# Optimization experiments

Measured on AMD Instinct MI355X. Metric: run time of the kernel, lower is better.

## Reference

```python
import jax, jax.numpy as jnp
import numpy as np

N = 131072      # points (rays x samples chunk)
E = 8           # spatial sub-networks (centroids)
DIN = 90        # encoded pos+dir features fed to sub-NeRFs (xyz_real=True -> x[:, 3:])
H = 256         # sub-NeRF hidden width
DOUT = 4        # rgb + sigma
MARGIN = 2.0    # boundary_margin
EPS = 1e-8


def setup_inputs() -> dict:
    key = jax.random.key(0)
    k = jax.random.split(key, 5)
    x_xyz = jax.random.uniform(k[0], (N, 3), dtype=jnp.float32)          # routing coords in [0,1)^3
    x_feat = jax.random.normal(k[1], (N, DIN), dtype=jnp.float32)        # encoded features
    x = jnp.concatenate([x_xyz, x_feat], axis=1)                         # [N, 3+DIN]
    centroids = jax.random.uniform(k[2], (E, 3), dtype=jnp.float32)
    W1 = jax.random.normal(k[3], (E, DIN, H), dtype=jnp.float32) * 0.05
    b1 = jnp.zeros((E, H), dtype=jnp.float32)
    W2 = jax.random.normal(k[4], (E, H, DOUT), dtype=jnp.float32) * 0.05
    b2 = jnp.zeros((E, DOUT), dtype=jnp.float32)
    return {"x": x, "centroids": centroids, "W1": W1, "b1": b1, "W2": W2, "b2": b2}


def reference(x, centroids, W1, b1, W2, b2):
    # --- centroid routing (torch.cdist equivalent) ---
    xyz = x[:, :3]                                                       # [N,3]
    d2 = jnp.sum((xyz[:, None, :] - centroids[None, :, :]) ** 2, axis=-1)
    dist = jnp.sqrt(jnp.maximum(d2, 0.0))                                # [N,E]
    inv = 1.0 / (dist + EPS)
    min_d = jnp.min(dist, axis=1, keepdims=True)                         # [N,1]
    inv = jnp.where(dist > MARGIN * min_d, 0.0, inv)                     # zero far experts
    weights = inv / jnp.sum(inv, axis=-1, keepdims=True)                 # [N,E], rows sum to 1

    # --- per-expert sub-NeRF MLP, weighted combine ---
    # Dense-equivalent of masked gather + weighted scatter-add: experts whose
    # weight is exactly 0 contribute nothing, matching the torch masked path.
    feat = x[:, 3:]                                                      # xyz_real=True -> drop xyz
    h = jax.nn.relu(jnp.einsum('nd,edh->enh', feat, W1) + b1[:, None, :])  # [E,N,H]
    out_e = jnp.einsum('enh,eho->eno', h, W2) + b2[:, None, :]             # [E,N,DOUT]
    return jnp.einsum('eno,ne->no', out_e, weights)                        # [N,DOUT]
```

## Files before the change

kernel.cpp:

```cpp
#include <hip/hip_runtime.h>

#define NPTS 131072
#define NE 8
#define DIN 90
#define NH 256

typedef __attribute__((ext_vector_type(8))) short bf16x8;
typedef __attribute__((ext_vector_type(4))) float f32x4;
typedef __attribute__((ext_vector_type(2))) float f32x2;
typedef __attribute__((ext_vector_type(4))) unsigned int u32x4;
typedef __attribute__((ext_vector_type(2))) unsigned int u32x2;
typedef __attribute__((ext_vector_type(4), aligned(4))) float f32x4a;
typedef __attribute__((ext_vector_type(2), aligned(4))) float f32x2a;

__device__ __forceinline__ unsigned short f2bf(float f) {
  unsigned int u = __float_as_uint(f);
  u += 0x7fffu + ((u >> 16) & 1u);
  return (unsigned short)(u >> 16);
}

#if defined(__has_builtin) && __has_builtin(__builtin_amdgcn_cvt_pk_bf16_f32)
typedef __attribute__((ext_vector_type(2))) __bf16 bf16x2;
__device__ __forceinline__ unsigned int pkbf(float f0, float f1) {
  bf16x2 r = __builtin_amdgcn_cvt_pk_bf16_f32(f0, f1);
  return __builtin_bit_cast(unsigned int, r);
}
#else
__device__ __forceinline__ unsigned int pkbf(float f0, float f1) {
  unsigned int u0 = __float_as_uint(f0) + 0x7fffu;
  unsigned int u1 = __float_as_uint(f1) + 0x7fffu;
  return __builtin_amdgcn_perm(u1, u0, 0x07060302u);
}
#endif

__device__ __forceinline__ bf16x8 cvt8(f32x4 a, f32x4 b) {
  u32x4 r;
  r[0] = pkbf(a[0], a[1]);
  r[1] = pkbf(a[2], a[3]);
  r[2] = pkbf(b[0], b[1]);
  r[3] = pkbf(b[2], b[3]);
  return __builtin_bit_cast(bf16x8, r);
}

#define PREP_T (184320 + 12288 + 8192 + 24576)
__global__ __launch_bounds__(256) void prep(const float* __restrict__ W1,
                                            const float* __restrict__ W2,
                                            unsigned short* __restrict__ W1T,
                                            unsigned short* __restrict__ W2T) {
  int tid = blockIdx.x * 256 + threadIdx.x;
  if (tid < 184320) {
    float v = W1[tid];
    int n = tid & 255, r = tid >> 8;
    int kp = r % 90, e = r / 90;
    W1T[(size_t)(e * NH + n) * 96 + kp] = f2bf(v);
    return;
  }
  tid -= 184320;
  if (tid < 12288) {
    int kp = 90 + tid % 6, q = tid / 6;
    int n = q & 255, e = q >> 8;
    W1T[(size_t)(e * NH + n) * 96 + kp] = 0;
    return;
  }
  tid -= 12288;
  if (tid < 8192) {
    float v = W2[tid];
    int o = tid & 3, k = (tid >> 2) & 255, e = tid >> 10;
    W2T[(size_t)(e * 16 + o) * NH + k] = f2bf(v);
    return;
  }
  tid -= 8192;
  if (tid < 24576) {
    int k = tid & 255, q = tid >> 8;
    int o = 4 + q % 12, e = q / 12;
    W2T[(size_t)(e * 16 + o) * NH + k] = 0;
  }
}

__global__ __launch_bounds__(256, 3) void meganerf_main(
    const float* __restrict__ x, const float* __restrict__ cent,
    const float* __restrict__ b1, const float* __restrict__ b2,
    const unsigned short* __restrict__ W1T, const unsigned short* __restrict__ W2T,
    float* __restrict__ out) {
  __shared__ unsigned short sH[4 * 2048];
  __shared__ float sW[NE][64];
  __shared__ float sB2[64][4];
  __shared__ float sB1[NE * NH];

  const int t    = threadIdx.x;
  const int lane = t & 63;
  const int wid  = t >> 6;
  const int l15  = lane & 15;
  const int l4   = lane >> 4;
  const int row0 = blockIdx.x * 64;
  const int gbase = wid * 2048;

#pragma unroll
  for (int j = 0; j < 2; ++j)
    *(f32x4*)&sB1[t * 4 + j * 1024] = *(const f32x4a*)&b1[t * 4 + j * 1024];

  bf16x8 bfr[4][3];
#pragma unroll
  for (int nf = 0; nf < 4; ++nf) {
    const float* gr = x + (size_t)(row0 + 16 * nf + l15) * 93 + 3;
    f32x4 v0, v1;
    v0 = *(const f32x4a*)(gr + 8 * l4);
    v1 = *(const f32x4a*)(gr + 8 * l4 + 4);
    bfr[nf][0] = cvt8(v0, v1);
    v0 = *(const f32x4a*)(gr + 32 + 8 * l4);
    v1 = *(const f32x4a*)(gr + 36 + 8 * l4);
    bfr[nf][1] = cvt8(v0, v1);
    if (l4 < 3) {
      v0 = *(const f32x4a*)(gr + 64 + 8 * l4);
      v1 = *(const f32x4a*)(gr + 68 + 8 * l4);
    } else {
      f32x2 tl = *(const f32x2a*)(gr + 88);
      v0[0] = tl[0]; v0[1] = tl[1]; v0[2] = 0.f; v0[3] = 0.f;
      v1[0] = 0.f; v1[1] = 0.f; v1[2] = 0.f; v1[3] = 0.f;
    }
    bfr[nf][2] = cvt8(v0, v1);
  }

  if (t < 64) {
    const float* gx = x + (size_t)(row0 + t) * 93;
    float px = gx[0], py = gx[1], pz = gx[2];
    float dist[NE], inv[NE];
    float mind = 3.4e38f;
#pragma unroll
    for (int e = 0; e < NE; ++e) {
      float dx = px - cent[e * 3 + 0];
      float dy = py - cent[e * 3 + 1];
      float dz = pz - cent[e * 3 + 2];
      float d2 = dx * dx + dy * dy + dz * dz;
      float d = sqrtf(fmaxf(d2, 0.f));
      dist[e] = d;
      inv[e] = 1.f / (d + 1e-8f);
      mind = fminf(mind, d);
    }
    float s = 0.f;
#pragma unroll
    for (int e = 0; e < NE; ++e) {
      if (dist[e] > 2.0f * mind) inv[e] = 0.f;
      s += inv[e];
    }
    float rs = 1.f / s;
    float bb[4] = {0.f, 0.f, 0.f, 0.f};
#pragma unroll
    for (int e = 0; e < NE; ++e) {
      float w = inv[e] * rs;
      sW[e][t] = w;
#pragma unroll
      for (int o = 0; o < 4; ++o) bb[o] += w * b2[e * 4 + o];
    }
#pragma unroll
    for (int o = 0; o < 4; ++o) sB2[t][o] = bb[o];
  }
  __syncthreads();

  bf16x8 w1buf[2][6];
  bf16x8 bwbuf[2];
  float wv[4];

  auto loadW1 = [&](int idx, int buf) {
    const int e = idx >> 1, c = idx & 1;
    const unsigned short* p =
        W1T + (size_t)(e * NH + 128 * c + 32 * wid + l15) * 96 + 8 * l4;
#pragma unroll
    for (int mf = 0; mf < 2; ++mf)
#pragma unroll
      for (int ks = 0; ks < 3; ++ks)
        w1buf[buf][mf * 3 + ks] = *(const bf16x8*)(p + mf * (16 * 96) + 32 * ks);
  };
  auto loadBW = [&](int idx, int buf) {
    const int e = idx >> 1, c = idx & 1;
    bwbuf[buf] = *(const bf16x8*)(W2T + (size_t)(e * 16 + l15) * NH +
                                  128 * c + 32 * wid + 8 * l4);
  };

  loadBW(0, 0);
  loadW1(0, 0);

  f32x4 facc[4] = {{0.f, 0.f, 0.f, 0.f}, {0.f, 0.f, 0.f, 0.f},
                   {0.f, 0.f, 0.f, 0.f}, {0.f, 0.f, 0.f, 0.f}};

#pragma unroll 2
  for (int i = 0; i < 16; ++i) {
    const int e = i >> 1, c = i & 1, cur = i & 1, nxt = cur ^ 1;
    const int colbase = 128 * c + 32 * wid;

    f32x4 b1v0 = *(const f32x4*)&sB1[e * NH + colbase + 4 * l4];
    f32x4 b1v1 = *(const f32x4*)&sB1[e * NH + colbase + 16 + 4 * l4];
    if (c == 0) {
#pragma unroll
      for (int nf = 0; nf < 4; ++nf) wv[nf] = sW[e][16 * nf + l15];
    }

    const int ip = (i + 1) & 15;
    loadBW(ip, nxt);
    loadW1(ip, nxt);

#pragma unroll
    for (int mf = 0; mf < 2; ++mf) {
      const f32x4 b1v = (mf == 0) ? b1v0 : b1v1;
      f32x4 acc[4];
#pragma unroll
      for (int nf = 0; nf < 4; ++nf)
        acc[nf] = __builtin_amdgcn_mfma_f32_16x16x32_bf16(
            w1buf[cur][mf * 3 + 0], bfr[nf][0], b1v, 0, 0, 0);
#pragma unroll
      for (int ks = 1; ks < 3; ++ks)
#pragma unroll
        for (int nf = 0; nf < 4; ++nf)
          acc[nf] = __builtin_amdgcn_mfma_f32_16x16x32_bf16(
              w1buf[cur][mf * 3 + ks], bfr[nf][ks], acc[nf], 0, 0, 0);

#pragma unroll
      for (int nf = 0; nf < 4; ++nf) {
        const float w = wv[nf];
        f32x4 a = acc[nf];
        f32x2 p0, p1;
        p0[0] = a[0]; p0[1] = a[1];
        p1[0] = a[2]; p1[1] = a[3];
        const f32x2 z = {0.f, 0.f};
        p0 = __builtin_elementwise_max(p0, z) * w;
        p1 = __builtin_elementwise_max(p1, z) * w;
        u32x2 pk;
        pk[0] = pkbf(p0[0], p0[1]);
        pk[1] = pkbf(p1[0], p1[1]);
        *(u32x2*)&sH[gbase + (nf * 64 + (l15 + 16 * (2 * mf + (l4 >> 1)))) * 8 +
                     4 * (l4 & 1)] = pk;
      }
    }

#pragma unroll
    for (int rf = 0; rf < 4; ++rf) {
      bf16x8 ah = *(const bf16x8*)&sH[gbase + (rf * 64 + lane) * 8];
      facc[rf] = __builtin_amdgcn_mfma_f32_16x16x32_bf16(ah, bwbuf[cur], facc[rf], 0, 0, 0);
    }
  }

  __syncthreads();
  float* sOutP = (float*)sH;
  if (l15 < 4) {
#pragma unroll
    for (int rf = 0; rf < 4; ++rf)
#pragma unroll
      for (int r = 0; r < 4; ++r)
        sOutP[(wid * 64 + 16 * rf + 4 * l4 + r) * 4 + l15] = facc[rf][r];
  }
  __syncthreads();
  {
    const int row = t >> 2, o = t & 3;
    float v = sB2[row][o] + sOutP[(0 * 64 + row) * 4 + o] + sOutP[(1 * 64 + row) * 4 + o] +
              sOutP[(2 * 64 + row) * 4 + o] + sOutP[(3 * 64 + row) * 4 + o];
    out[row0 * 4 + t] = v;
  }
}

extern "C" void kernel_launch(void* const* d_in, const int* in_sizes, int n_in,
                              void* d_out, int out_size, void* d_ws, size_t ws_size,
                              hipStream_t stream) {
  const float* x    = (const float*)d_in[0];
  const float* cent = (const float*)d_in[1];
  const float* W1   = (const float*)d_in[2];
  const float* b1   = (const float*)d_in[3];
  const float* W2   = (const float*)d_in[4];
  const float* b2   = (const float*)d_in[5];
  float* out = (float*)d_out;

  unsigned short* W1T = (unsigned short*)d_ws;
  unsigned short* W2T = W1T + NE * NH * 96;

  prep<<<(PREP_T + 255) / 256, 256, 0, stream>>>(W1, W2, W1T, W2T);
  meganerf_main<<<NPTS / 64, 256, 0, stream>>>(x, cent, b1, b2, W1T, W2T, out);
}
```

Baseline: 163.1 us.

## Route points to experts and run sparse per-expert GEMMs with atomic combine

Replaces the dense all-experts-per-point MLP with a routing pass that builds a per-expert list of points whose weight is nonzero, then launches per-expert tiles that gather those rows, run the two-layer MLP for that expert only, scale by the routing weight, and atomically add into a zeroed output. The aim is to skip MLP work for experts masked out by the boundary margin. In exchange it adds a routing kernel, two memsets, gathered non-contiguous row loads, float atomics on the output, and a launch of 16384 blocks where most exit early. The speedup depends on how many experts survive the margin test per point.

```diff
diff --git a/kernel.cpp b/kernel.cpp
--- a/kernel.cpp
+++ b/kernel.cpp
@@ -4,6 +4,8 @@
 #define NE 8
 #define DIN 90
 #define NH 256
+#define TILES 2048
+#define NBLK (NE * TILES)
 
 typedef __attribute__((ext_vector_type(8))) short bf16x8;
 typedef __attribute__((ext_vector_type(4))) float f32x4;
@@ -40,6 +42,31 @@
   r[2] = pkbf(b[0], b[1]);
   r[3] = pkbf(b[2], b[3]);
   return __builtin_bit_cast(bf16x8, r);
+}
+
+__device__ __forceinline__ void expert_w(const float* __restrict__ cent,
+                                         float px, float py, float pz,
+                                         float* inv, float* s_out) {
+  float dist[NE];
+  float mind = 3.4e38f;
+#pragma unroll
+  for (int e = 0; e < NE; ++e) {
+    float dx = px - cent[e * 3 + 0];
+    float dy = py - cent[e * 3 + 1];
+    float dz = pz - cent[e * 3 + 2];
+    float d2 = dx * dx + dy * dy + dz * dz;
+    float d = sqrtf(fmaxf(d2, 0.f));
+    dist[e] = d;
+    mind = fminf(mind, d);
+  }
+  float s = 0.f;
+#pragma unroll
+  for (int e = 0; e < NE; ++e) {
+    float iv = (dist[e] <= 2.0f * mind) ? 1.f / (dist[e] + 1e-8f) : 0.f;
+    inv[e] = iv;
+    s += iv;
+  }
+  *s_out = s;
 }
 
 #define PREP_T (184320 + 12288 + 8192 + 24576)
@@ -77,32 +104,70 @@
   }
 }
 
-__global__ __launch_bounds__(256, 3) void meganerf_main(
+__global__ __launch_bounds__(256) void route(const float* __restrict__ x,
+                                             const float* __restrict__ cent,
+                                             int* __restrict__ cnt,
+                                             int* __restrict__ idxList) {
+  const int n = blockIdx.x * 256 + threadIdx.x;
+  const int lane = threadIdx.x & 63;
+  f32x4 p = *(const f32x4a*)(x + (size_t)n * 93);
+  float inv[NE], s;
+  expert_w(cent, p[0], p[1], p[2], inv, &s);
+#pragma unroll
+  for (int e = 0; e < NE; ++e) {
+    bool pred = inv[e] > 0.f;
+    unsigned long long m = __ballot(pred);
+    if (m) {
+      int leader = __ffsll((unsigned long long)m) - 1;
+      int base = 0;
+      if (lane == leader) base = atomicAdd(&cnt[e], __popcll(m));
+      base = __shfl(base, leader, 64);
+      if (pred)
+        idxList[(size_t)e * NPTS + base + __popcll(m & ((1ull << lane) - 1ull))] = n;
+    }
+  }
+}
+
+__global__ __launch_bounds__(256, 3) void expert_gemm(
     const float* __restrict__ x, const float* __restrict__ cent,
     const float* __restrict__ b1, const float* __restrict__ b2,
     const unsigned short* __restrict__ W1T, const unsigned short* __restrict__ W2T,
+    const int* __restrict__ cnt, const int* __restrict__ idxList,
     float* __restrict__ out) {
+  const int e = blockIdx.x >> 11;
+  const int tile = blockIdx.x & (TILES - 1);
+  const int start = tile * 64;
+  const int cn = cnt[e];
+  if (start >= cn) return;
+
   __shared__ unsigned short sH[4 * 2048];
-  __shared__ float sW[NE][64];
-  __shared__ float sB2[64][4];
-  __shared__ float sB1[NE * NH];
+  __shared__ int sRow[64];
+  __shared__ float sWloc[64];
 
   const int t    = threadIdx.x;
   const int lane = t & 63;
   const int wid  = t >> 6;
   const int l15  = lane & 15;
   const int l4   = lane >> 4;
-  const int row0 = blockIdx.x * 64;
   const int gbase = wid * 2048;
 
-#pragma unroll
-  for (int j = 0; j < 2; ++j)
-    *(f32x4*)&sB1[t * 4 + j * 1024] = *(const f32x4a*)&b1[t * 4 + j * 1024];
+  if (t < 64) {
+    const int slot = start + t;
+    const int sl = (slot < cn) ? slot : start;
+    const int n = idxList[(size_t)e * NPTS + sl];
+    const float* gx = x + (size_t)n * 93;
+    float inv[NE], s;
+    expert_w(cent, gx[0], gx[1], gx[2], inv, &s);
+    sRow[t] = n;
+    sWloc[t] = (slot < cn) ? inv[e] / s : 0.f;
+  }
+  __syncthreads();
 
   bf16x8 bfr[4][3];
 #pragma unroll
   for (int nf = 0; nf < 4; ++nf) {
-    const float* gr = x + (size_t)(row0 + 16 * nf + l15) * 93 + 3;
+    const int n = sRow[16 * nf + l15];
+    const float* gr = x + (size_t)n * 93 + 3;
     f32x4 v0, v1;
     v0 = *(const f32x4a*)(gr + 8 * l4);
     v1 = *(const f32x4a*)(gr + 8 * l4 + 4);
@@ -121,48 +186,9 @@
     bfr[nf][2] = cvt8(v0, v1);
   }
 
-  if (t < 64) {
-    const float* gx = x + (size_t)(row0 + t) * 93;
-    float px = gx[0], py = gx[1], pz = gx[2];
-    float dist[NE], inv[NE];
-    float mind = 3.4e38f;
-#pragma unroll
-    for (int e = 0; e < NE; ++e) {
-      float dx = px - cent[e * 3 + 0];
-      float dy = py - cent[e * 3 + 1];
-      float dz = pz - cent[e * 3 + 2];
-      float d2 = dx * dx + dy * dy + dz * dz;
-      float d = sqrtf(fmaxf(d2, 0.f));
-      dist[e] = d;
-      inv[e] = 1.f / (d + 1e-8f);
-      mind = fminf(mind, d);
-    }
-    float s = 0.f;
-#pragma unroll
-    for (int e = 0; e < NE; ++e) {
-      if (dist[e] > 2.0f * mind) inv[e] = 0.f;
-      s += inv[e];
-    }
-    float rs = 1.f / s;
-    float bb[4] = {0.f, 0.f, 0.f, 0.f};
-#pragma unroll
-    for (int e = 0; e < NE; ++e) {
-      float w = inv[e] * rs;
-      sW[e][t] = w;
-#pragma unroll
-      for (int o = 0; o < 4; ++o) bb[o] += w * b2[e * 4 + o];
-    }
-#pragma unroll
-    for (int o = 0; o < 4; ++o) sB2[t][o] = bb[o];
-  }
-  __syncthreads();
-
   bf16x8 w1buf[2][6];
-  bf16x8 bwbuf[2];
-  float wv[4];
-
-  auto loadW1 = [&](int idx, int buf) {
-    const int e = idx >> 1, c = idx & 1;
+  bf16x8 bwb[2];
+  auto loadW1 = [&](int c, int buf) {
     const unsigned short* p =
         W1T + (size_t)(e * NH + 128 * c + 32 * wid + l15) * 96 + 8 * l4;
 #pragma unroll
@@ -171,33 +197,26 @@
       for (int ks = 0; ks < 3; ++ks)
         w1buf[buf][mf * 3 + ks] = *(const bf16x8*)(p + mf * (16 * 96) + 32 * ks);
   };
-  auto loadBW = [&](int idx, int buf) {
-    const int e = idx >> 1, c = idx & 1;
-    bwbuf[buf] = *(const bf16x8*)(W2T + (size_t)(e * 16 + l15) * NH +
-                                  128 * c + 32 * wid + 8 * l4);
+  auto loadBW = [&](int c, int buf) {
+    bwb[buf] = *(const bf16x8*)(W2T + (size_t)(e * 16 + l15) * NH +
+                                128 * c + 32 * wid + 8 * l4);
   };
-
   loadBW(0, 0);
   loadW1(0, 0);
 
-  f32x4 facc[4] = {{0.f, 0.f, 0.f, 0.f}, {0.f, 0.f, 0.f, 0.f},
-                   {0.f, 0.f, 0.f, 0.f}, {0.f, 0.f, 0.f, 0.f}};
-
-#pragma unroll 2
-  for (int i = 0; i < 16; ++i) {
-    const int e = i >> 1, c = i & 1, cur = i & 1, nxt = cur ^ 1;
+  const float b2v = (wid == 0 && l15 < 4) ? b2[e * 4 + l15] : 0.f;
+  f32x4 facc[4];
+#pragma unroll
+  for (int rf = 0; rf < 4; ++rf)
+#pragma unroll
+    for (int r = 0; r < 4; ++r) facc[rf][r] = b2v;
+
+#pragma unroll
+  for (int c = 0; c < 2; ++c) {
+    if (c == 0) { loadBW(1, 1); loadW1(1, 1); }
     const int colbase = 128 * c + 32 * wid;
-
-    f32x4 b1v0 = *(const f32x4*)&sB1[e * NH + colbase + 4 * l4];
-    f32x4 b1v1 = *(const f32x4*)&sB1[e * NH + colbase + 16 + 4 * l4];
-    if (c == 0) {
-#pragma unroll
-      for (int nf = 0; nf < 4; ++nf) wv[nf] = sW[e][16 * nf + l15];
-    }
-
-    const int ip = (i + 1) & 15;
-    loadBW(ip, nxt);
-    loadW1(ip, nxt);
+    f32x4 b1v0 = *(const f32x4a*)(b1 + e * NH + colbase + 4 * l4);
+    f32x4 b1v1 = *(const f32x4a*)(b1 + e * NH + colbase + 16 + 4 * l4);
 
 #pragma unroll
     for (int mf = 0; mf < 2; ++mf) {
@@ -206,27 +225,20 @@
 #pragma unroll
       for (int nf = 0; nf < 4; ++nf)
         acc[nf] = __builtin_amdgcn_mfma_f32_16x16x32_bf16(
-            w1buf[cur][mf * 3 + 0], bfr[nf][0], b1v, 0, 0, 0);
+            w1buf[c][mf * 3 + 0], bfr[nf][0], b1v, 0, 0, 0);
 #pragma unroll
       for (int ks = 1; ks < 3; ++ks)
 #pragma unroll
         for (int nf = 0; nf < 4; ++nf)
           acc[nf] = __builtin_amdgcn_mfma_f32_16x16x32_bf16(
-              w1buf[cur][mf * 3 + ks], bfr[nf][ks], acc[nf], 0, 0, 0);
+              w1buf[c][mf * 3 + ks], bfr[nf][ks], acc[nf], 0, 0, 0);
 
 #pragma unroll
       for (int nf = 0; nf < 4; ++nf) {
-        const float w = wv[nf];
         f32x4 a = acc[nf];
-        f32x2 p0, p1;
-        p0[0] = a[0]; p0[1] = a[1];
-        p1[0] = a[2]; p1[1] = a[3];
-        const f32x2 z = {0.f, 0.f};
-        p0 = __builtin_elementwise_max(p0, z) * w;
-        p1 = __builtin_elementwise_max(p1, z) * w;
         u32x2 pk;
-        pk[0] = pkbf(p0[0], p0[1]);
-        pk[1] = pkbf(p1[0], p1[1]);
+        pk[0] = pkbf(fmaxf(a[0], 0.f), fmaxf(a[1], 0.f));
+        pk[1] = pkbf(fmaxf(a[2], 0.f), fmaxf(a[3], 0.f));
         *(u32x2*)&sH[gbase + (nf * 64 + (l15 + 16 * (2 * mf + (l4 >> 1)))) * 8 +
                      4 * (l4 & 1)] = pk;
       }
@@ -235,9 +247,15 @@
 #pragma unroll
     for (int rf = 0; rf < 4; ++rf) {
       bf16x8 ah = *(const bf16x8*)&sH[gbase + (rf * 64 + lane) * 8];
-      facc[rf] = __builtin_amdgcn_mfma_f32_16x16x32_bf16(ah, bwbuf[cur], facc[rf], 0, 0, 0);
-    }
-  }
+      facc[rf] = __builtin_amdgcn_mfma_f32_16x16x32_bf16(ah, bwb[c], facc[rf], 0, 0, 0);
+    }
+  }
+
+#pragma unroll
+  for (int rf = 0; rf < 4; ++rf)
+#pragma unroll
+    for (int r = 0; r < 4; ++r)
+      facc[rf][r] *= sWloc[16 * rf + 4 * l4 + r];
 
   __syncthreads();
   float* sOutP = (float*)sH;
@@ -251,9 +269,9 @@
   __syncthreads();
   {
     const int row = t >> 2, o = t & 3;
-    float v = sB2[row][o] + sOutP[(0 * 64 + row) * 4 + o] + sOutP[(1 * 64 + row) * 4 + o] +
+    float v = sOutP[(0 * 64 + row) * 4 + o] + sOutP[(1 * 64 + row) * 4 + o] +
               sOutP[(2 * 64 + row) * 4 + o] + sOutP[(3 * 64 + row) * 4 + o];
-    out[row0 * 4 + t] = v;
+    atomicAdd(&out[(size_t)sRow[row] * 4 + o], v);
   }
 }
 
@@ -270,7 +288,12 @@
 
   unsigned short* W1T = (unsigned short*)d_ws;
   unsigned short* W2T = W1T + NE * NH * 96;
-
+  int* cnt     = (int*)((char*)d_ws + 458752);
+  int* idxList = (int*)((char*)d_ws + 458816);
+
+  hipMemsetAsync(cnt, 0, 64, stream);
+  hipMemsetAsync(out, 0, (size_t)NPTS * 4 * sizeof(float), stream);
   prep<<<(PREP_T + 255) / 256, 256, 0, stream>>>(W1, W2, W1T, W2T);
-  meganerf_main<<<NPTS / 64, 256, 0, stream>>>(x, cent, b1, b2, W1T, W2T, out);
-}
+  route<<<NPTS / 256, 256, 0, stream>>>(x, cent, cnt, idxList);
+  expert_gemm<<<NBLK, 256, 0, stream>>>(x, cent, b1, b2, W1T, W2T, cnt, idxList, out);
+}
```

Result: slower. 384.0 us (+135.5%).

## Software-pipeline second-layer MFMA one step behind using double-buffered LDS hidden tile

Applied to the files above, without the earlier changes.

The second-layer MFMA for chunk i-1 is deferred and interleaved with the first-layer MFMAs of chunk i. The hidden tile in LDS is double-buffered so the next chunk's writes do not overwrite data still being read. Register double-buffering of W1/W2 prefetch is dropped in favour of direct loads at use, and b1 is read straight from global memory instead of being staged in LDS. This aims to hide LDS write-read latency, but larger LDS use may cut occupancy and the global loads are no longer prefetched ahead.

```diff
diff --git a/kernel.cpp b/kernel.cpp
--- a/kernel.cpp
+++ b/kernel.cpp
@@ -82,10 +82,9 @@
     const float* __restrict__ b1, const float* __restrict__ b2,
     const unsigned short* __restrict__ W1T, const unsigned short* __restrict__ W2T,
     float* __restrict__ out) {
-  __shared__ unsigned short sH[4 * 2048];
+  __shared__ unsigned short sH[8 * 4096];
   __shared__ float sW[NE][64];
   __shared__ float sB2[64][4];
-  __shared__ float sB1[NE * NH];
 
   const int t    = threadIdx.x;
   const int lane = t & 63;
@@ -93,11 +92,7 @@
   const int l15  = lane & 15;
   const int l4   = lane >> 4;
   const int row0 = blockIdx.x * 64;
-  const int gbase = wid * 2048;
-
-#pragma unroll
-  for (int j = 0; j < 2; ++j)
-    *(f32x4*)&sB1[t * 4 + j * 1024] = *(const f32x4a*)&b1[t * 4 + j * 1024];
+  const int gbase = wid * 4096;
 
   bf16x8 bfr[4][3];
 #pragma unroll
@@ -157,47 +152,43 @@
   }
   __syncthreads();
 
-  bf16x8 w1buf[2][6];
-  bf16x8 bwbuf[2];
-  float wv[4];
-
-  auto loadW1 = [&](int idx, int buf) {
-    const int e = idx >> 1, c = idx & 1;
-    const unsigned short* p =
-        W1T + (size_t)(e * NH + 128 * c + 32 * wid + l15) * 96 + 8 * l4;
-#pragma unroll
-    for (int mf = 0; mf < 2; ++mf)
-#pragma unroll
-      for (int ks = 0; ks < 3; ++ks)
-        w1buf[buf][mf * 3 + ks] = *(const bf16x8*)(p + mf * (16 * 96) + 32 * ks);
-  };
-  auto loadBW = [&](int idx, int buf) {
-    const int e = idx >> 1, c = idx & 1;
-    bwbuf[buf] = *(const bf16x8*)(W2T + (size_t)(e * 16 + l15) * NH +
-                                  128 * c + 32 * wid + 8 * l4);
-  };
-
-  loadBW(0, 0);
-  loadW1(0, 0);
-
   f32x4 facc[4] = {{0.f, 0.f, 0.f, 0.f}, {0.f, 0.f, 0.f, 0.f},
                    {0.f, 0.f, 0.f, 0.f}, {0.f, 0.f, 0.f, 0.f}};
+  float wv[4];
 
 #pragma unroll 2
   for (int i = 0; i < 16; ++i) {
-    const int e = i >> 1, c = i & 1, cur = i & 1, nxt = cur ^ 1;
+    const int e = i >> 1, c = i & 1;
+    const int cur = i & 1, prev = cur ^ 1;
     const int colbase = 128 * c + 32 * wid;
 
-    f32x4 b1v0 = *(const f32x4*)&sB1[e * NH + colbase + 4 * l4];
-    f32x4 b1v1 = *(const f32x4*)&sB1[e * NH + colbase + 16 + 4 * l4];
+    bf16x8 ah[4];
+    bf16x8 bwp;
+    if (i > 0) {
+      const int ep = (i - 1) >> 1, cp = (i - 1) & 1;
+#pragma unroll
+      for (int rf = 0; rf < 4; ++rf)
+        ah[rf] = *(const bf16x8*)&sH[gbase + prev * 2048 + (rf * 64 + lane) * 8];
+      bwp = *(const bf16x8*)(W2T + (size_t)(ep * 16 + l15) * NH +
+                             128 * cp + 32 * wid + 8 * l4);
+    }
+
+    f32x4 b1v0 = *(const f32x4a*)(b1 + e * NH + colbase + 4 * l4);
+    f32x4 b1v1 = *(const f32x4a*)(b1 + e * NH + colbase + 16 + 4 * l4);
+    bf16x8 w1f[6];
+    {
+      const unsigned short* p =
+          W1T + (size_t)(e * NH + colbase + l15) * 96 + 8 * l4;
+#pragma unroll
+      for (int mf = 0; mf < 2; ++mf)
+#pragma unroll
+        for (int ks = 0; ks < 3; ++ks)
+          w1f[mf * 3 + ks] = *(const bf16x8*)(p + mf * (16 * 96) + 32 * ks);
+    }
     if (c == 0) {
 #pragma unroll
       for (int nf = 0; nf < 4; ++nf) wv[nf] = sW[e][16 * nf + l15];
     }
-
-    const int ip = (i + 1) & 15;
-    loadBW(ip, nxt);
-    loadW1(ip, nxt);
 
 #pragma unroll
     for (int mf = 0; mf < 2; ++mf) {
@@ -206,13 +197,19 @@
 #pragma unroll
       for (int nf = 0; nf < 4; ++nf)
         acc[nf] = __builtin_amdgcn_mfma_f32_16x16x32_bf16(
-            w1buf[cur][mf * 3 + 0], bfr[nf][0], b1v, 0, 0, 0);
+            w1f[mf * 3 + 0], bfr[nf][0], b1v, 0, 0, 0);
 #pragma unroll
       for (int ks = 1; ks < 3; ++ks)
 #pragma unroll
         for (int nf = 0; nf < 4; ++nf)
           acc[nf] = __builtin_amdgcn_mfma_f32_16x16x32_bf16(
-              w1buf[cur][mf * 3 + ks], bfr[nf][ks], acc[nf], 0, 0, 0);
+              w1f[mf * 3 + ks], bfr[nf][ks], acc[nf], 0, 0, 0);
+
+      if (mf == 0 && i > 0) {
+#pragma unroll
+        for (int rf = 0; rf < 4; ++rf)
+          facc[rf] = __builtin_amdgcn_mfma_f32_16x16x32_bf16(ah[rf], bwp, facc[rf], 0, 0, 0);
+      }
 
 #pragma unroll
       for (int nf = 0; nf < 4; ++nf) {
@@ -227,15 +224,20 @@
         u32x2 pk;
         pk[0] = pkbf(p0[0], p0[1]);
         pk[1] = pkbf(p1[0], p1[1]);
-        *(u32x2*)&sH[gbase + (nf * 64 + (l15 + 16 * (2 * mf + (l4 >> 1)))) * 8 +
+        *(u32x2*)&sH[gbase + cur * 2048 +
+                     (nf * 64 + (l15 + 16 * (2 * mf + (l4 >> 1)))) * 8 +
                      4 * (l4 & 1)] = pk;
       }
     }
-
+  }
+
+  {
+    bf16x8 bwp = *(const bf16x8*)(W2T + (size_t)(7 * 16 + l15) * NH +
+                                  128 + 32 * wid + 8 * l4);
 #pragma unroll
     for (int rf = 0; rf < 4; ++rf) {
-      bf16x8 ah = *(const bf16x8*)&sH[gbase + (rf * 64 + lane) * 8];
-      facc[rf] = __builtin_amdgcn_mfma_f32_16x16x32_bf16(ah, bwbuf[cur], facc[rf], 0, 0, 0);
+      bf16x8 ah = *(const bf16x8*)&sH[gbase + 2048 + (rf * 64 + lane) * 8];
+      facc[rf] = __builtin_amdgcn_mfma_f32_16x16x32_bf16(ah, bwp, facc[rf], 0, 0, 0);
     }
   }
 
```

Measured after the change: 173.0 us. 6.1% more time.
